# Optimization experiments

Measured on AMD Instinct MI355X. Metric: run time of the kernel, lower is better.

The kernel has to match this reference:

```python
import jax, jax.numpy as jnp
import numpy as np

DIM_LATENT = 256
NUM_ATOM_TYPES = 16
NUM_EDGE_TYPES = 4
HIDDEN = 256
HIDDEN_FINAL = 256
BS, N = 8, 256


def setup_inputs() -> dict:
    key = jax.random.key(0)
    ks = jax.random.split(key, 12)
    s = lambda fan_in: 1.0 / np.sqrt(fan_in)
    return {
        "latent": jax.random.normal(ks[0], (BS, N, DIM_LATENT), jnp.float32),
        "positions": jax.random.normal(ks[1], (BS, N, 3), jnp.float32),
        "atom_types": jax.random.uniform(ks[2], (BS, N, NUM_ATOM_TYPES), jnp.float32),
        # latent_mlp: Linear(dim_latent, hidden) -> ReLU -> Linear(hidden, hidden)
        "W1": jax.random.uniform(ks[3], (DIM_LATENT, HIDDEN), jnp.float32, -s(DIM_LATENT), s(DIM_LATENT)),
        "b1": jax.random.uniform(ks[4], (HIDDEN,), jnp.float32, -s(DIM_LATENT), s(DIM_LATENT)),
        "W2": jax.random.uniform(ks[5], (HIDDEN, HIDDEN), jnp.float32, -s(HIDDEN), s(HIDDEN)),
        "b2": jax.random.uniform(ks[6], (HIDDEN,), jnp.float32, -s(HIDDEN), s(HIDDEN)),
        # final_mlp: Linear(1+num_atom_types+dim_latent, hidden_final) -> ReLU -> Linear(hidden_final, num_edge_types)
        "W3": jax.random.uniform(ks[7], (1 + NUM_ATOM_TYPES + DIM_LATENT, HIDDEN_FINAL), jnp.float32, -s(1 + NUM_ATOM_TYPES + DIM_LATENT), s(1 + NUM_ATOM_TYPES + DIM_LATENT)),
        "b3": jax.random.uniform(ks[8], (HIDDEN_FINAL,), jnp.float32, -s(1 + NUM_ATOM_TYPES + DIM_LATENT), s(1 + NUM_ATOM_TYPES + DIM_LATENT)),
        "W4": jax.random.uniform(ks[9], (HIDDEN_FINAL, NUM_EDGE_TYPES), jnp.float32, -s(HIDDEN_FINAL), s(HIDDEN_FINAL)),
        "b4": jax.random.uniform(ks[10], (NUM_EDGE_TYPES,), jnp.float32, -s(HIDDEN_FINAL), s(HIDDEN_FINAL)),
    }


def _pairwise_dist(positions):
    # torch.cdist (euclidean), grad-safe sqrt (zero on the diagonal)
    diff = positions[:, :, None, :] - positions[:, None, :, :]  # bs x n x n x 3
    d2 = jnp.sum(diff * diff, axis=-1)
    safe = jnp.where(d2 > 0, d2, 1.0)
    return jnp.where(d2 > 0, jnp.sqrt(safe), 0.0)


def reference(latent, positions, atom_types, W1, b1, W2, b2, W3, b3, W4, b4):
    # latent_mlp
    h = jax.nn.relu(latent @ W1 + b1) @ W2 + b2  # bs x n x hidden (== dim_latent)
    dist = _pairwise_dist(positions)[..., None]  # bs x n x n x 1
    atom_pairs = atom_types[:, :, None, :] * atom_types[:, None, :, :]  # bs x n x n x A
    latent_pairs = h[:, :, None, :] * h[:, None, :, :]                  # bs x n x n x C
    y = jnp.concatenate((dist, atom_pairs, latent_pairs), axis=3)
    return jax.nn.relu(y @ W3 + b3) @ W4 + b4  # bs x n x n x num_edge_types
```

## Files before the change

kernel.cpp:

```cpp
#include <hip/hip_runtime.h>

#define DIM 256
#define NA 16
#define NE 4
#define KTOT 288

typedef __attribute__((ext_vector_type(8))) short short8;
typedef __attribute__((ext_vector_type(4))) float f32x4;

static __device__ __forceinline__ ushort f2bf(float f) {
  union { float f; unsigned int u; } v; v.f = f;
  unsigned int r = (v.u + 0x7FFFu + ((v.u >> 16) & 1u)) >> 16;
  return (ushort)r;
}

static __device__ __forceinline__ float bf2f(ushort s) {
  union { unsigned int u; float f; } v; v.u = ((unsigned int)s) << 16;
  return v.f;
}

static __device__ __forceinline__ unsigned cvtpk(float lo, float hi) {
  unsigned r;
  asm("v_cvt_pk_bf16_f32 %0, %1, %2" : "=v"(r) : "v"(lo), "v"(hi));
  return r;
}

static __device__ __forceinline__ int fragIdx(int row, int c) {
  return (((row >> 4)*9 + (c >> 5))*4 + ((c >> 3) & 3))*128 + (row & 15)*8 + (c & 7);
}

__global__ __launch_bounds__(256) void prep_h_kernel(
    const float* __restrict__ latent, const float* __restrict__ atoms,
    const float* __restrict__ W1, const float* __restrict__ b1,
    const float* __restrict__ W2, const float* __restrict__ b2,
    ushort* __restrict__ Gf) {
  __shared__ float lat[8][DIM];
  __shared__ float t1[8][DIM];
  const int b = blockIdx.x >> 5, i0 = (blockIdx.x & 31) * 8;
  const int k = threadIdx.x;
  #pragma unroll
  for (int r = 0; r < 8; ++r) lat[r][k] = latent[(b*256 + i0 + r) * DIM + k];
  __syncthreads();
  float acc[8];
  #pragma unroll
  for (int r = 0; r < 8; ++r) acc[r] = b1[k];
  for (int c = 0; c < DIM; c += 4) {
    float w0 = W1[(c+0)*DIM + k], w1 = W1[(c+1)*DIM + k];
    float w2 = W1[(c+2)*DIM + k], w3 = W1[(c+3)*DIM + k];
    #pragma unroll
    for (int r = 0; r < 8; ++r) {
      const float4 l4 = *reinterpret_cast<const float4*>(&lat[r][c]);
      acc[r] += l4.x*w0 + l4.y*w1 + l4.z*w2 + l4.w*w3;
    }
  }
  #pragma unroll
  for (int r = 0; r < 8; ++r) t1[r][k] = fmaxf(acc[r], 0.f);
  __syncthreads();
  #pragma unroll
  for (int r = 0; r < 8; ++r) acc[r] = b2[k];
  for (int c = 0; c < DIM; c += 4) {
    float w0 = W2[(c+0)*DIM + k], w1 = W2[(c+1)*DIM + k];
    float w2 = W2[(c+2)*DIM + k], w3 = W2[(c+3)*DIM + k];
    #pragma unroll
    for (int r = 0; r < 8; ++r) {
      const float4 l4 = *reinterpret_cast<const float4*>(&t1[r][c]);
      acc[r] += l4.x*w0 + l4.y*w1 + l4.z*w2 + l4.w*w3;
    }
  }
  #pragma unroll
  for (int r = 0; r < 8; ++r) {
    int row = b*256 + i0 + r;
    Gf[fragIdx(row, NA + k)] = f2bf(acc[r]);
  }
  if (k < NA) {
    #pragma unroll
    for (int r = 0; r < 8; ++r) {
      int row = b*256 + i0 + r;
      Gf[fragIdx(row, k)] = f2bf(atoms[row*NA + k]);
      Gf[fragIdx(row, 272 + k)] = 0;
    }
  }
}

__global__ __launch_bounds__(256) void prep_w3t_kernel(
    const float* __restrict__ W3, ushort* __restrict__ W3Tf) {
  const int n = blockIdx.x, c = threadIdx.x;
  W3Tf[fragIdx(n, c)] = (c < 272) ? f2bf(W3[(1+c)*DIM + n]) : (ushort)0;
  if (c < 32) {
    int c2 = 256 + c;
    W3Tf[fragIdx(n, c2)] = (c2 < 272) ? f2bf(W3[(1+c2)*DIM + n]) : (ushort)0;
  }
}

__global__ __attribute__((amdgpu_flat_work_group_size(512,512), amdgpu_waves_per_eu(2,2)))
void edge_main_kernel(
    const float* __restrict__ positions,
    const float* __restrict__ W3, const float* __restrict__ b3,
    const float* __restrict__ W4, const float* __restrict__ b4,
    const ushort* __restrict__ Gf, const ushort* __restrict__ W3Tf,
    float* __restrict__ out) {
  __shared__ ushort gi_lds[4608];
  __shared__ ushort gj_lds[4608];
  __shared__ float partial[4][256][4];
  __shared__ float dist_lds[256];

  const int bid = blockIdx.x;
  const int b = bid / 136;
  int q = bid - b*136;
  int it = 0;
  while (q >= 16 - it) { q -= 16 - it; ++it; }
  const int jt = it + q;
  const int i0 = b*256 + it*16, j0 = b*256 + jt*16;
  const int rbi = i0 >> 4, rbj = j0 >> 4;

  const int tid = threadIdx.x;
  const int lane = tid & 63, w = tid >> 6;
  const int wn = w & 3;
  const int wp = w >> 2;
  const int c15 = lane & 15, hi = lane >> 4;

  {
    const uint4* srcI = reinterpret_cast<const uint4*>(Gf + (size_t)rbi*4608);
    const uint4* srcJ = reinterpret_cast<const uint4*>(Gf + (size_t)rbj*4608);
    uint4* dI = reinterpret_cast<uint4*>(gi_lds);
    uint4* dJ = reinterpret_cast<uint4*>(gj_lds);
    dI[tid] = srcI[tid];
    dJ[tid] = srcJ[tid];
    if (tid < 64) { dI[512+tid] = srcI[512+tid]; dJ[512+tid] = srcJ[512+tid]; }
  }
  if (tid < 256) {
    int pi = tid >> 4, pj = tid & 15;
    const float* pa = &positions[(i0 + pi)*3];
    const float* pb = &positions[(j0 + pj)*3];
    float dx = pa[0]-pb[0], dy = pa[1]-pb[1], dz = pa[2]-pb[2];
    float d2 = dx*dx + dy*dy + dz*dz;
    dist_lds[tid] = d2 > 0.f ? sqrtf(d2) : 0.f;
  }
  __syncthreads();

  f32x4 acc[4][8];
  #pragma unroll
  for (int at = 0; at < 4; ++at)
    #pragma unroll
    for (int bt = 0; bt < 8; ++bt) { acc[at][bt].x=0.f; acc[at][bt].y=0.f; acc[at][bt].z=0.f; acc[at][bt].w=0.f; }

  #pragma unroll
  for (int kk = 0; kk < 9; ++kk) {
    short8 afr[4];
    #pragma unroll
    for (int at = 0; at < 4; ++at)
      afr[at] = *reinterpret_cast<const short8*>(
          &W3Tf[((wn*4 + at)*9 + kk)*512 + lane*8]);
    union { ushort us[8]; short8 s8; } gj;
    gj.s8 = *reinterpret_cast<const short8*>(&gj_lds[kk*512 + lane*8]);
    float gjf[8];
    #pragma unroll
    for (int s = 0; s < 8; ++s) gjf[s] = bf2f(gj.us[s]);
    #pragma unroll
    for (int bt = 0; bt < 8; ++bt) {
      int ptg = wp*8 + bt;
      union { ushort us[8]; short8 s8; } gi;
      gi.s8 = *reinterpret_cast<const short8*>(
          &gi_lds[kk*512 + hi*128 + ptg*8]);
      union { unsigned uu[4]; short8 s8; } bb;
      bb.uu[0] = cvtpk(bf2f(gi.us[0])*gjf[0], bf2f(gi.us[1])*gjf[1]);
      bb.uu[1] = cvtpk(bf2f(gi.us[2])*gjf[2], bf2f(gi.us[3])*gjf[3]);
      bb.uu[2] = cvtpk(bf2f(gi.us[4])*gjf[4], bf2f(gi.us[5])*gjf[5]);
      bb.uu[3] = cvtpk(bf2f(gi.us[6])*gjf[6], bf2f(gi.us[7])*gjf[7]);
      acc[0][bt] = __builtin_amdgcn_mfma_f32_16x16x32_bf16(afr[0], bb.s8, acc[0][bt], 0, 0, 0);
      acc[1][bt] = __builtin_amdgcn_mfma_f32_16x16x32_bf16(afr[1], bb.s8, acc[1][bt], 0, 0, 0);
      acc[2][bt] = __builtin_amdgcn_mfma_f32_16x16x32_bf16(afr[2], bb.s8, acc[2][bt], 0, 0, 0);
      acc[3][bt] = __builtin_amdgcn_mfma_f32_16x16x32_bf16(afr[3], bb.s8, acc[3][bt], 0, 0, 0);
    }
  }

  __builtin_amdgcn_sched_barrier(0);

  float4 pe[8];
  #pragma unroll
  for (int bt = 0; bt < 8; ++bt) { pe[bt].x=0.f; pe[bt].y=0.f; pe[bt].z=0.f; pe[bt].w=0.f; }
  #pragma unroll
  for (int at = 0; at < 4; ++at) {
    float b3v[4], w30v[4]; float4 w4v[4];
    #pragma unroll
    for (int r = 0; r < 4; ++r) {
      int n = (wn*4 + at)*16 + hi*4 + r;
      b3v[r]  = b3[n];
      w30v[r] = W3[n];
      w4v[r]  = *reinterpret_cast<const float4*>(&W4[n*4]);
    }
    #pragma unroll
    for (int bt = 0; bt < 8; ++bt) {
      float d = dist_lds[(wp*8 + bt)*16 + c15];
      #pragma unroll
      for (int r = 0; r < 4; ++r) {
        float z  = acc[at][bt][r] + d*w30v[r] + b3v[r];
        float rz = fmaxf(z, 0.f);
        pe[bt].x += rz*w4v[r].x; pe[bt].y += rz*w4v[r].y;
        pe[bt].z += rz*w4v[r].z; pe[bt].w += rz*w4v[r].w;
      }
    }
  }
  #pragma unroll
  for (int bt = 0; bt < 8; ++bt) {
    int pair = (wp*8 + bt)*16 + c15;
    float4 p = pe[bt];
    p.x += __shfl_xor(p.x, 16); p.y += __shfl_xor(p.y, 16);
    p.z += __shfl_xor(p.z, 16); p.w += __shfl_xor(p.w, 16);
    p.x += __shfl_xor(p.x, 32); p.y += __shfl_xor(p.y, 32);
    p.z += __shfl_xor(p.z, 32); p.w += __shfl_xor(p.w, 32);
    if (hi == 0) *reinterpret_cast<float4*>(&partial[wn][pair][0]) = p;
  }
  __syncthreads();
  if (tid < 256) {
    int pair = tid;
    float4 v;
    v.x = partial[0][pair][0] + partial[1][pair][0] + partial[2][pair][0] + partial[3][pair][0];
    v.y = partial[0][pair][1] + partial[1][pair][1] + partial[2][pair][1] + partial[3][pair][1];
    v.z = partial[0][pair][2] + partial[1][pair][2] + partial[2][pair][2] + partial[3][pair][2];
    v.w = partial[0][pair][3] + partial[1][pair][3] + partial[2][pair][3] + partial[3][pair][3];
    const float4 bv = *reinterpret_cast<const float4*>(b4);
    v.x += bv.x; v.y += bv.y; v.z += bv.z; v.w += bv.w;
    int il = it*16 + (pair >> 4);
    int jl = jt*16 + (pair & 15);
    *reinterpret_cast<float4*>(&out[(((size_t)b*256 + il)*256 + jl)*NE]) = v;
    if (it != jt)
      *reinterpret_cast<float4*>(&out[(((size_t)b*256 + jl)*256 + il)*NE]) = v;
  }
}

extern "C" void kernel_launch(void* const* d_in, const int* in_sizes, int n_in,
                              void* d_out, int out_size, void* d_ws, size_t ws_size,
                              hipStream_t stream) {
  const float* latent    = (const float*)d_in[0];
  const float* positions = (const float*)d_in[1];
  const float* atoms     = (const float*)d_in[2];
  const float* W1 = (const float*)d_in[3];
  const float* b1 = (const float*)d_in[4];
  const float* W2 = (const float*)d_in[5];
  const float* b2 = (const float*)d_in[6];
  const float* W3 = (const float*)d_in[7];
  const float* b3 = (const float*)d_in[8];
  const float* W4 = (const float*)d_in[9];
  const float* b4 = (const float*)d_in[10];
  float* out = (float*)d_out;

  char* ws = (char*)d_ws;
  ushort* Gf_ws   = (ushort*)ws;
  ushort* W3Tf_ws = (ushort*)(ws + 1179648);

  hipLaunchKernelGGL(prep_h_kernel, dim3(256), dim3(256), 0, stream,
                     latent, atoms, W1, b1, W2, b2, Gf_ws);
  hipLaunchKernelGGL(prep_w3t_kernel, dim3(256), dim3(256), 0, stream, W3, W3Tf_ws);
  hipLaunchKernelGGL(edge_main_kernel, dim3(1088), dim3(512), 0, stream,
                     positions, W3, b3, W4, b4, Gf_ws, W3Tf_ws, out);
}
```

Before: 100.7 us.

## Split each 16x16 edge tile across four smaller 256-thread blocks

Each 16x16 pair tile is now split into four sub-blocks of 4 i-rows, launched as 4352 blocks of 256 threads instead of 1088 blocks of 512. Each wave keeps all four accumulator tiles but covers four pair groups instead of eight, and occupancy is raised to three waves per EU. The MFMA loop is reordered so the B fragments are built first and each W3 fragment is loaded once and used across four MFMAs. The cost is that every block still loads the full gi and gj tiles into LDS, so global-to-LDS traffic for those tiles roughly quadruples in exchange for more parallelism and less register pressure.

New measurement: 100.3 us. About the same (-0.4%).

```diff
diff --git a/kernel.cpp b/kernel.cpp
--- a/kernel.cpp
+++ b/kernel.cpp
@@ -92,7 +92,7 @@
   }
 }
 
-__global__ __attribute__((amdgpu_flat_work_group_size(512,512), amdgpu_waves_per_eu(2,2)))
+__global__ __attribute__((amdgpu_flat_work_group_size(256,256), amdgpu_waves_per_eu(3,3)))
 void edge_main_kernel(
     const float* __restrict__ positions,
     const float* __restrict__ W3, const float* __restrict__ b3,
@@ -101,12 +101,14 @@
     float* __restrict__ out) {
   __shared__ ushort gi_lds[4608];
   __shared__ ushort gj_lds[4608];
-  __shared__ float partial[4][256][4];
-  __shared__ float dist_lds[256];
+  __shared__ float partial[4][64][4];
+  __shared__ float dist_lds[64];
 
   const int bid = blockIdx.x;
-  const int b = bid / 136;
-  int q = bid - b*136;
+  const int b = bid / 544;
+  int rem = bid - b*544;
+  const int qq4 = rem & 3;
+  int q = rem >> 2;
   int it = 0;
   while (q >= 16 - it) { q -= 16 - it; ++it; }
   const int jt = it + q;
@@ -115,8 +117,6 @@
 
   const int tid = threadIdx.x;
   const int lane = tid & 63, w = tid >> 6;
-  const int wn = w & 3;
-  const int wp = w >> 2;
   const int c15 = lane & 15, hi = lane >> 4;
 
   {
@@ -126,72 +126,76 @@
     uint4* dJ = reinterpret_cast<uint4*>(gj_lds);
     dI[tid] = srcI[tid];
     dJ[tid] = srcJ[tid];
+    dI[256+tid] = srcI[256+tid];
+    dJ[256+tid] = srcJ[256+tid];
     if (tid < 64) { dI[512+tid] = srcI[512+tid]; dJ[512+tid] = srcJ[512+tid]; }
   }
-  if (tid < 256) {
+  if (tid < 64) {
     int pi = tid >> 4, pj = tid & 15;
-    const float* pa = &positions[(i0 + pi)*3];
+    const float* pa = &positions[(i0 + qq4*4 + pi)*3];
     const float* pb = &positions[(j0 + pj)*3];
     float dx = pa[0]-pb[0], dy = pa[1]-pb[1], dz = pa[2]-pb[2];
     float d2 = dx*dx + dy*dy + dz*dz;
     dist_lds[tid] = d2 > 0.f ? sqrtf(d2) : 0.f;
   }
-  __syncthreads();
-
-  f32x4 acc[4][8];
+
+  f32x4 acc[4][4];
   #pragma unroll
   for (int at = 0; at < 4; ++at)
     #pragma unroll
-    for (int bt = 0; bt < 8; ++bt) { acc[at][bt].x=0.f; acc[at][bt].y=0.f; acc[at][bt].z=0.f; acc[at][bt].w=0.f; }
+    for (int bt = 0; bt < 4; ++bt) { acc[at][bt].x=0.f; acc[at][bt].y=0.f; acc[at][bt].z=0.f; acc[at][bt].w=0.f; }
+
+  __syncthreads();
 
   #pragma unroll
   for (int kk = 0; kk < 9; ++kk) {
-    short8 afr[4];
-    #pragma unroll
-    for (int at = 0; at < 4; ++at)
-      afr[at] = *reinterpret_cast<const short8*>(
-          &W3Tf[((wn*4 + at)*9 + kk)*512 + lane*8]);
     union { ushort us[8]; short8 s8; } gj;
     gj.s8 = *reinterpret_cast<const short8*>(&gj_lds[kk*512 + lane*8]);
     float gjf[8];
     #pragma unroll
     for (int s = 0; s < 8; ++s) gjf[s] = bf2f(gj.us[s]);
-    #pragma unroll
-    for (int bt = 0; bt < 8; ++bt) {
-      int ptg = wp*8 + bt;
+    short8 bbv[4];
+    #pragma unroll
+    for (int bt = 0; bt < 4; ++bt) {
       union { ushort us[8]; short8 s8; } gi;
       gi.s8 = *reinterpret_cast<const short8*>(
-          &gi_lds[kk*512 + hi*128 + ptg*8]);
+          &gi_lds[kk*512 + hi*128 + (qq4*4 + bt)*8]);
       union { unsigned uu[4]; short8 s8; } bb;
       bb.uu[0] = cvtpk(bf2f(gi.us[0])*gjf[0], bf2f(gi.us[1])*gjf[1]);
       bb.uu[1] = cvtpk(bf2f(gi.us[2])*gjf[2], bf2f(gi.us[3])*gjf[3]);
       bb.uu[2] = cvtpk(bf2f(gi.us[4])*gjf[4], bf2f(gi.us[5])*gjf[5]);
       bb.uu[3] = cvtpk(bf2f(gi.us[6])*gjf[6], bf2f(gi.us[7])*gjf[7]);
-      acc[0][bt] = __builtin_amdgcn_mfma_f32_16x16x32_bf16(afr[0], bb.s8, acc[0][bt], 0, 0, 0);
-      acc[1][bt] = __builtin_amdgcn_mfma_f32_16x16x32_bf16(afr[1], bb.s8, acc[1][bt], 0, 0, 0);
-      acc[2][bt] = __builtin_amdgcn_mfma_f32_16x16x32_bf16(afr[2], bb.s8, acc[2][bt], 0, 0, 0);
-      acc[3][bt] = __builtin_amdgcn_mfma_f32_16x16x32_bf16(afr[3], bb.s8, acc[3][bt], 0, 0, 0);
+      bbv[bt] = bb.s8;
+    }
+    #pragma unroll
+    for (int at = 0; at < 4; ++at) {
+      short8 af = *reinterpret_cast<const short8*>(
+          &W3Tf[((w*4 + at)*9 + kk)*512 + lane*8]);
+      acc[at][0] = __builtin_amdgcn_mfma_f32_16x16x32_bf16(af, bbv[0], acc[at][0], 0, 0, 0);
+      acc[at][1] = __builtin_amdgcn_mfma_f32_16x16x32_bf16(af, bbv[1], acc[at][1], 0, 0, 0);
+      acc[at][2] = __builtin_amdgcn_mfma_f32_16x16x32_bf16(af, bbv[2], acc[at][2], 0, 0, 0);
+      acc[at][3] = __builtin_amdgcn_mfma_f32_16x16x32_bf16(af, bbv[3], acc[at][3], 0, 0, 0);
     }
   }
 
   __builtin_amdgcn_sched_barrier(0);
 
-  float4 pe[8];
-  #pragma unroll
-  for (int bt = 0; bt < 8; ++bt) { pe[bt].x=0.f; pe[bt].y=0.f; pe[bt].z=0.f; pe[bt].w=0.f; }
+  float4 pe[4];
+  #pragma unroll
+  for (int bt = 0; bt < 4; ++bt) { pe[bt].x=0.f; pe[bt].y=0.f; pe[bt].z=0.f; pe[bt].w=0.f; }
   #pragma unroll
   for (int at = 0; at < 4; ++at) {
     float b3v[4], w30v[4]; float4 w4v[4];
     #pragma unroll
     for (int r = 0; r < 4; ++r) {
-      int n = (wn*4 + at)*16 + hi*4 + r;
+      int n = (w*4 + at)*16 + hi*4 + r;
       b3v[r]  = b3[n];
       w30v[r] = W3[n];
       w4v[r]  = *reinterpret_cast<const float4*>(&W4[n*4]);
     }
     #pragma unroll
-    for (int bt = 0; bt < 8; ++bt) {
-      float d = dist_lds[(wp*8 + bt)*16 + c15];
+    for (int bt = 0; bt < 4; ++bt) {
+      float d = dist_lds[bt*16 + c15];
       #pragma unroll
       for (int r = 0; r < 4; ++r) {
         float z  = acc[at][bt][r] + d*w30v[r] + b3v[r];
@@ -202,17 +206,17 @@
     }
   }
   #pragma unroll
-  for (int bt = 0; bt < 8; ++bt) {
-    int pair = (wp*8 + bt)*16 + c15;
+  for (int bt = 0; bt < 4; ++bt) {
+    int pair = bt*16 + c15;
     float4 p = pe[bt];
     p.x += __shfl_xor(p.x, 16); p.y += __shfl_xor(p.y, 16);
     p.z += __shfl_xor(p.z, 16); p.w += __shfl_xor(p.w, 16);
     p.x += __shfl_xor(p.x, 32); p.y += __shfl_xor(p.y, 32);
     p.z += __shfl_xor(p.z, 32); p.w += __shfl_xor(p.w, 32);
-    if (hi == 0) *reinterpret_cast<float4*>(&partial[wn][pair][0]) = p;
-  }
-  __syncthreads();
-  if (tid < 256) {
+    if (hi == 0) *reinterpret_cast<float4*>(&partial[w][pair][0]) = p;
+  }
+  __syncthreads();
+  if (tid < 64) {
     int pair = tid;
     float4 v;
     v.x = partial[0][pair][0] + partial[1][pair][0] + partial[2][pair][0] + partial[3][pair][0];
@@ -221,7 +225,7 @@
     v.w = partial[0][pair][3] + partial[1][pair][3] + partial[2][pair][3] + partial[3][pair][3];
     const float4 bv = *reinterpret_cast<const float4*>(b4);
     v.x += bv.x; v.y += bv.y; v.z += bv.z; v.w += bv.w;
-    int il = it*16 + (pair >> 4);
+    int il = it*16 + qq4*4 + (pair >> 4);
     int jl = jt*16 + (pair & 15);
     *reinterpret_cast<float4*>(&out[(((size_t)b*256 + il)*256 + jl)*NE]) = v;
     if (it != jt)
@@ -252,6 +256,6 @@
   hipLaunchKernelGGL(prep_h_kernel, dim3(256), dim3(256), 0, stream,
                      latent, atoms, W1, b1, W2, b2, Gf_ws);
   hipLaunchKernelGGL(prep_w3t_kernel, dim3(256), dim3(256), 0, stream, W3, W3Tf_ws);
-  hipLaunchKernelGGL(edge_main_kernel, dim3(1088), dim3(512), 0, stream,
+  hipLaunchKernelGGL(edge_main_kernel, dim3(4352), dim3(256), 0, stream,
                      positions, W3, b3, W4, b4, Gf_ws, W3Tf_ws, out);
 }
```
